# Kernel optimization log

Hardware: AMD Instinct MI355X
Metric: run time of the kernel (lower is better)

Reference implementation:

```python
import jax, jax.numpy as jnp
import numpy as np

N = 50000
E = 800000
IN, HID, OUT = 256, 128, 64
NEG_SLOPE = 0.2


def _gat(x, src, dst, W, a_src, a_dst, b, heads, dim, concat):
    # PyG GATConv (eval mode, self-loops already appended to src/dst)
    xh = (x @ W).reshape(N, heads, dim)              # [N,H,D]
    s_src = jnp.einsum('nhd,hd->nh', xh, a_src)       # [N,H]
    s_dst = jnp.einsum('nhd,hd->nh', xh, a_dst)
    e = jax.nn.leaky_relu(s_src[src] + s_dst[dst], NEG_SLOPE)  # [Etot,H]
    m = jax.ops.segment_max(e, dst, num_segments=N)
    e = jnp.exp(e - m[dst])
    z = jax.ops.segment_sum(e, dst, num_segments=N)
    alpha = e / z[dst]                                # segment softmax over incoming edges
    msg = xh[src] * alpha[:, :, None]                 # [Etot,H,D] gather + weight
    out = jax.ops.segment_sum(msg, dst, num_segments=N)  # scatter-add aggregate
    out = out.reshape(N, heads * dim) if concat else out.mean(axis=1)
    return out + b


def setup_inputs():
    key = jax.random.key(0)
    ks = jax.random.split(key, 20)
    sc = 0.05
    inp = {
        'x': jax.random.normal(ks[0], (N, IN), jnp.float32),
        'edge_index': jax.random.randint(ks[1], (2, E), 0, N, jnp.int64) if jax.config.read('jax_enable_x64') else jax.random.randint(ks[1], (2, E), 0, N, jnp.int32),
        # semantic MLP
        'w1': jax.random.normal(ks[2], (IN, HID), jnp.float32) * sc,
        'b1': jnp.zeros((HID,), jnp.float32),
        'w2': jax.random.normal(ks[3], (HID, HID), jnp.float32) * sc,
        'b2': jnp.zeros((HID,), jnp.float32),
        # gat1: HID -> HID//2, heads=4, concat -> 2*HID
        'g1_w': jax.random.normal(ks[4], (HID, 4 * (HID // 2)), jnp.float32) * sc,
        'g1_asrc': jax.random.normal(ks[5], (4, HID // 2), jnp.float32) * sc,
        'g1_adst': jax.random.normal(ks[6], (4, HID // 2), jnp.float32) * sc,
        'g1_b': jnp.zeros((2 * HID,), jnp.float32),
        # gat2: 2*HID -> OUT, heads=2, mean
        'g2_w': jax.random.normal(ks[7], (2 * HID, 2 * OUT), jnp.float32) * sc,
        'g2_asrc': jax.random.normal(ks[8], (2, OUT), jnp.float32) * sc,
        'g2_adst': jax.random.normal(ks[9], (2, OUT), jnp.float32) * sc,
        'g2_b': jnp.zeros((OUT,), jnp.float32),
        # gat3: OUT -> OUT, heads=1, mean
        'g3_w': jax.random.normal(ks[10], (OUT, OUT), jnp.float32) * sc,
        'g3_asrc': jax.random.normal(ks[11], (1, OUT), jnp.float32) * sc,
        'g3_adst': jax.random.normal(ks[12], (1, OUT), jnp.float32) * sc,
        'g3_b': jnp.zeros((OUT,), jnp.float32),
    }
    return inp


def reference(x, edge_index, w1, b1, w2, b2,
              g1_w, g1_asrc, g1_adst, g1_b,
              g2_w, g2_asrc, g2_adst, g2_b,
              g3_w, g3_asrc, g3_adst, g3_b):
    # add self loops once (PyG GATConv default add_self_loops=True)
    loop = jnp.arange(N, dtype=edge_index.dtype)
    src = jnp.concatenate([edge_index[0], loop])
    dst = jnp.concatenate([edge_index[1], loop])
    # semantic MLP (eval: dropout is identity)
    h = jax.nn.relu(x @ w1 + b1)
    h = jax.nn.relu(h @ w2 + b2)
    h = jax.nn.elu(_gat(h, src, dst, g1_w, g1_asrc, g1_adst, g1_b, 4, HID // 2, True))
    h = jax.nn.elu(_gat(h, src, dst, g2_w, g2_asrc, g2_adst, g2_b, 2, OUT, False))
    h = _gat(h, src, dst, g3_w, g3_asrc, g3_adst, g3_b, 1, OUT, False)
    return h
```

## Files before the change

### kernel.cpp

```cpp
#include <hip/hip_runtime.h>
#include <hip/hip_fp16.h>
#include <math.h>

#define NN 50000
#define NE 800000

static inline int ceil_div_h(int a, int b) { return (a + b - 1) / b; }

typedef _Float16 half8 __attribute__((ext_vector_type(8)));
typedef float f32x4 __attribute__((ext_vector_type(4)));

__global__ __launch_bounds__(256)
void prep_kernel(const float* __restrict__ w1, const float* __restrict__ w2,
                 const float* __restrict__ g1w, const float* __restrict__ g2w,
                 const float* __restrict__ g3w, __half* __restrict__ wt,
                 int* __restrict__ cursor) {
  int idx = blockIdx.x * 256 + threadIdx.x;
  if (idx < NN) cursor[idx] = 0;
  const float* W; int K, N, li;
  if (idx < 32768)        { W = w1;  K = 256; N = 128; li = idx; }
  else if (idx < 49152)   { W = w2;  K = 128; N = 128; li = idx - 32768; }
  else if (idx < 81920)   { W = g1w; K = 128; N = 256; li = idx - 49152; }
  else if (idx < 114688)  { W = g2w; K = 256; N = 128; li = idx - 81920; }
  else if (idx < 118784)  { W = g3w; K = 64;  N = 64;  li = idx - 114688; }
  else return;
  int n = li / K, k = li - n * K;
  wt[idx] = __float2half_rn(W[(size_t)k * N + n]);
}

template<int BM, int TN, int WR, int WC, int ACT, int OUTH, int AF32, int HS>
__global__ __launch_bounds__(256)
void mfma_gemm(const void* __restrict__ Av, const __half* __restrict__ Bt,
               const float* __restrict__ bias, void* __restrict__ Cv,
               const float* __restrict__ a_src, const float* __restrict__ a_dst,
               float* __restrict__ s_src, float* __restrict__ s_dst,
               int M, int N, int K) {
  constexpr int FM = BM / WR / 16;
  constexpr int FN = TN / WC / 16;
  constexpr int SA = 40;
  __shared__ __align__(16) _Float16 As[BM * SA];
  __shared__ __align__(16) _Float16 Bs[TN * SA];
  const int tid = threadIdx.x;
  const int bm = blockIdx.y * BM, bn = blockIdx.x * TN;
  const int wave = tid >> 6, lane = tid & 63;
  const int wm = (wave % WR) * (BM / WR);
  const int wn = (wave / WR) * (TN / WC);
  const int l16 = lane & 15, quad = lane >> 4;

  f32x4 acc[FM][FN] = {};

  for (int k0 = 0; k0 < K; k0 += 32) {
    if (AF32) {
      const float* A = (const float*)Av;
      #pragma unroll
      for (int i = 0; i < (BM * 8) / 256; ++i) {
        int idx = tid + i * 256;
        int m = idx >> 3, q = idx & 7;
        int gm = bm + m;
        float4 v = make_float4(0.f, 0.f, 0.f, 0.f);
        if (gm < M) v = *(const float4*)&A[(size_t)gm * K + k0 + q * 4];
        union { __half2 h2[2]; float2 f2; } u;
        u.h2[0] = __floats2half2_rn(v.x, v.y);
        u.h2[1] = __floats2half2_rn(v.z, v.w);
        *(float2*)&As[m * SA + q * 4] = u.f2;
      }
    } else {
      const __half* A = (const __half*)Av;
      #pragma unroll
      for (int i = 0; i < (BM * 4) / 256; ++i) {
        int idx = tid + i * 256;
        int m = idx >> 2, q = (idx & 3) * 8;
        int gm = bm + m;
        float4 raw = make_float4(0.f, 0.f, 0.f, 0.f);
        if (gm < M) raw = *(const float4*)&A[(size_t)gm * K + k0 + q];
        *(float4*)&As[m * SA + q] = raw;
      }
    }
    #pragma unroll
    for (int i = 0; i < (TN * 4) / 256; ++i) {
      int idx = tid + i * 256;
      int n = idx >> 2, kq = (idx & 3) * 8;
      float4 raw = *(const float4*)&Bt[(size_t)(bn + n) * K + k0 + kq];
      *(float4*)&Bs[n * SA + kq] = raw;
    }
    __syncthreads();
    half8 af[FM], bf[FN];
    #pragma unroll
    for (int mi = 0; mi < FM; ++mi)
      af[mi] = *(const half8*)&As[(wm + mi * 16 + l16) * SA + quad * 8];
    #pragma unroll
    for (int ni = 0; ni < FN; ++ni)
      bf[ni] = *(const half8*)&Bs[(wn + ni * 16 + l16) * SA + quad * 8];
    #pragma unroll
    for (int mi = 0; mi < FM; ++mi)
      #pragma unroll
      for (int ni = 0; ni < FN; ++ni)
        acc[mi][ni] = __builtin_amdgcn_mfma_f32_16x16x32_f16(af[mi], bf[ni], acc[mi][ni], 0, 0, 0);
    __syncthreads();
  }

  #pragma unroll
  for (int mi = 0; mi < FM; ++mi) {
    #pragma unroll
    for (int r = 0; r < 4; ++r) {
      int gm = bm + wm + mi * 16 + quad * 4 + r;
      if (gm >= M) continue;
      #pragma unroll
      for (int ni = 0; ni < FN; ++ni) {
        int gn = bn + wn + ni * 16 + l16;
        float v = acc[mi][ni][r];
        if (bias) v += bias[gn];
        if (ACT == 1) v = fmaxf(v, 0.f);
        if (OUTH) ((__half*)Cv)[(size_t)gm * N + gn] = __float2half_rn(v);
        else      ((float*)Cv)[(size_t)gm * N + gn] = v;
      }
    }
  }

  if (HS > 0) {
    const int h = (bn + wn) >> 6;
    float asv[FN], adv[FN];
    #pragma unroll
    for (int ni = 0; ni < FN; ++ni) {
      int d = ni * 16 + l16;
      asv[ni] = a_src[h * 64 + d];
      adv[ni] = a_dst[h * 64 + d];
    }
    #pragma unroll
    for (int mi = 0; mi < FM; ++mi) {
      #pragma unroll
      for (int r = 0; r < 4; ++r) {
        float ss = 0.f, sd = 0.f;
        #pragma unroll
        for (int ni = 0; ni < FN; ++ni) {
          float v = acc[mi][ni][r];
          ss = fmaf(v, asv[ni], ss);
          sd = fmaf(v, adv[ni], sd);
        }
        #pragma unroll
        for (int off = 1; off < 16; off <<= 1) {
          ss += __shfl_xor(ss, off, 64);
          sd += __shfl_xor(sd, off, 64);
        }
        int gm = bm + wm + mi * 16 + quad * 4 + r;
        if (l16 == 0 && gm < M) {
          s_src[gm * HS + h] = ss;
          s_dst[gm * HS + h] = sd;
        }
      }
    }
  }
}


__global__ __launch_bounds__(256)
void hist_kernel(const int* __restrict__ ei, int* __restrict__ cnt) {
  int e = blockIdx.x * blockDim.x + threadIdx.x;
  if (e >= NE) return;
  atomicAdd(&cnt[ei[NE + e]], 1);
}

__global__ __launch_bounds__(256)
void scan1_kernel(const int* __restrict__ in, int* __restrict__ out,
                  int* __restrict__ bsum, int n) {
  __shared__ int tmp[256];
  int t = threadIdx.x;
  int i = blockIdx.x * 256 + t;
  int v = (i < n) ? in[i] : 0;
  tmp[t] = v;
  __syncthreads();
  for (int off = 1; off < 256; off <<= 1) {
    int u = (t >= off) ? tmp[t - off] : 0;
    __syncthreads();
    tmp[t] += u;
    __syncthreads();
  }
  if (i <= n) out[i] = tmp[t] - v;
  if (t == 255) bsum[blockIdx.x] = tmp[255];
}

__global__ __launch_bounds__(256)
void scan2_kernel(int* __restrict__ data, int n) {
  __shared__ int tmp[256];
  int t = threadIdx.x;
  int v = (t < n) ? data[t] : 0;
  tmp[t] = v;
  __syncthreads();
  for (int off = 1; off < 256; off <<= 1) {
    int u = (t >= off) ? tmp[t - off] : 0;
    __syncthreads();
    tmp[t] += u;
    __syncthreads();
  }
  if (t < n) data[t] = tmp[t] - v;
}

__global__ __launch_bounds__(256)
void scan3_kernel(int* __restrict__ out, const int* __restrict__ bsum,
                  int* __restrict__ cursor, int n) {
  int i = blockIdx.x * 256 + threadIdx.x;
  if (i > n) return;
  int v = out[i] + bsum[blockIdx.x];
  out[i] = v;
  if (i < n) cursor[i] = v;
}

__global__ __launch_bounds__(256)
void scatter_kernel(const int* __restrict__ ei, int* __restrict__ cursor,
                    int* __restrict__ srcs) {
  int e = blockIdx.x * blockDim.x + threadIdx.x;
  if (e >= NE) return;
  int s = ei[e], d = ei[NE + e];
  int pos = atomicAdd(&cursor[d], 1);
  srcs[pos] = s;
}

template<int H, int MODE>
__global__ __launch_bounds__(256)
void gat_aggregate(const int* __restrict__ rowptr, const int* __restrict__ srcs,
                   const float* __restrict__ ssrc, const float* __restrict__ sdst,
                   const __half* __restrict__ xh, const float* __restrict__ bias,
                   void* __restrict__ outv) {
  constexpr int HD = H * 64;
  __shared__ float wbuf[4][64 * H];
  __shared__ int sbuf[4][64];
  const int wslot = threadIdx.x >> 6;
  const int wid = (blockIdx.x * blockDim.x + threadIdx.x) >> 6;
  const int lane = threadIdx.x & 63;
  if (wid >= NN) return;
  const int n = wid;
  const int start = rowptr[n];
  const int end = rowptr[n + 1];
  const int h = (lane * H) >> 6;

  float sdv[H];
  #pragma unroll
  for (int hh = 0; hh < H; ++hh) sdv[hh] = sdst[n * H + hh];

  float z;
  float acc[H];
  {
    float wself[H];
    #pragma unroll
    for (int hh = 0; hh < H; ++hh) {
      float e = ssrc[n * H + hh] + sdv[hh];
      e = e >= 0.f ? e : 0.2f * e;
      wself[hh] = __expf(e);
    }
    float ws = wself[h];
    z = ws;
    const __half* xr = xh + (size_t)n * HD + lane * H;
    if (H == 4) {
      float2 raw = *(const float2*)xr;
      __half2 p0 = *(__half2*)&raw.x;
      __half2 p1 = *(__half2*)&raw.y;
      float2 f0 = __half22float2(p0), f1 = __half22float2(p1);
      acc[0] = ws * f0.x; acc[1] = ws * f0.y; acc[2] = ws * f1.x; acc[3] = ws * f1.y;
    } else if (H == 2) {
      float2 f0 = __half22float2(*(const __half2*)xr);
      acc[0] = ws * f0.x; acc[1] = ws * f0.y;
    } else {
      acc[0] = ws * __half2float(xr[0]);
    }
  }

  for (int base = start; base < end; base += 64) {
    int cnt = end - base;
    if (cnt > 64) cnt = 64;
    if (lane < cnt) {
      int s = srcs[base + lane];
      sbuf[wslot][lane] = s;
      float ev[H];
      if (H == 4) {
        float4 t = *(const float4*)&ssrc[s * 4];
        ev[0] = t.x; ev[1] = t.y; ev[2] = t.z; ev[3] = t.w;
      } else if (H == 2) {
        float2 t = *(const float2*)&ssrc[s * 2];
        ev[0] = t.x; ev[1] = t.y;
      } else {
        ev[0] = ssrc[s];
      }
      #pragma unroll
      for (int hh = 0; hh < H; ++hh) {
        float e = ev[hh] + sdv[hh];
        e = e >= 0.f ? e : 0.2f * e;
        wbuf[wslot][lane * H + hh] = __expf(e);
      }
    }
    #pragma unroll 4
    for (int j = 0; j < cnt; ++j) {
      int s = sbuf[wslot][j];
      float w = wbuf[wslot][j * H + h];
      z += w;
      const __half* xr = xh + (size_t)s * HD + lane * H;
      if (H == 4) {
        float2 raw = *(const float2*)xr;
        __half2 p0 = *(__half2*)&raw.x;
        __half2 p1 = *(__half2*)&raw.y;
        float2 f0 = __half22float2(p0), f1 = __half22float2(p1);
        acc[0] = fmaf(w, f0.x, acc[0]); acc[1] = fmaf(w, f0.y, acc[1]);
        acc[2] = fmaf(w, f1.x, acc[2]); acc[3] = fmaf(w, f1.y, acc[3]);
      } else if (H == 2) {
        float2 f0 = __half22float2(*(const __half2*)xr);
        acc[0] = fmaf(w, f0.x, acc[0]); acc[1] = fmaf(w, f0.y, acc[1]);
      } else {
        acc[0] = fmaf(w, __half2float(xr[0]), acc[0]);
      }
    }
  }
  const float inv = 1.f / z;

  if (MODE == 0) {
    __half* out = (__half*)outv;
    float v[4];
    #pragma unroll
    for (int i = 0; i < 4; ++i) {
      v[i] = acc[i] * inv + bias[lane * 4 + i];
      v[i] = v[i] > 0.f ? v[i] : expm1f(v[i]);
    }
    union { __half2 h2[2]; float2 f2; } u;
    u.h2[0] = __floats2half2_rn(v[0], v[1]);
    u.h2[1] = __floats2half2_rn(v[2], v[3]);
    *(float2*)&out[(size_t)n * 256 + lane * 4] = u.f2;
  } else if (MODE == 1) {
    __half* out = (__half*)outv;
    float sv[2];
    #pragma unroll
    for (int i = 0; i < 2; ++i) {
      float mine = acc[i] * inv;
      float other = __shfl_xor(mine, 32, 64);
      sv[i] = (mine + other) * 0.5f;
    }
    if (lane < 32) {
      float v0 = sv[0] + bias[lane * 2 + 0];
      float v1 = sv[1] + bias[lane * 2 + 1];
      v0 = v0 > 0.f ? v0 : expm1f(v0);
      v1 = v1 > 0.f ? v1 : expm1f(v1);
      *(__half2*)&out[(size_t)n * 64 + lane * 2] = __floats2half2_rn(v0, v1);
    }
  } else {
    float* out = (float*)outv;
    out[(size_t)n * 64 + lane] = acc[0] * inv + bias[lane];
  }
}


extern "C" void kernel_launch(void* const* d_in, const int* in_sizes, int n_in,
                              void* d_out, int out_size, void* d_ws, size_t ws_size,
                              hipStream_t stream) {
  const float* x    = (const float*)d_in[0];
  const int*   ei   = (const int*)d_in[1];
  const float* w1   = (const float*)d_in[2];
  const float* b1   = (const float*)d_in[3];
  const float* w2   = (const float*)d_in[4];
  const float* b2   = (const float*)d_in[5];
  const float* g1w  = (const float*)d_in[6];
  const float* g1as = (const float*)d_in[7];
  const float* g1ad = (const float*)d_in[8];
  const float* g1b  = (const float*)d_in[9];
  const float* g2w  = (const float*)d_in[10];
  const float* g2as = (const float*)d_in[11];
  const float* g2ad = (const float*)d_in[12];
  const float* g2b  = (const float*)d_in[13];
  const float* g3w  = (const float*)d_in[14];
  const float* g3as = (const float*)d_in[15];
  const float* g3ad = (const float*)d_in[16];
  const float* g3b  = (const float*)d_in[17];
  float* out = (float*)d_out;

  float* ws   = (float*)d_ws;
  float* bufA = ws;
  float* bufB = bufA + (size_t)NN * 256;
  float* bufC = bufB + (size_t)NN * 256;
  float* ssrc = bufC + (size_t)NN * 256;
  float* sdst = ssrc + (size_t)NN * 4;
  int* rowptr = (int*)(sdst + (size_t)NN * 4);
  int* cursor = rowptr + (NN + 1);
  int* bsum   = cursor + NN;
  int* srcs   = bsum + 256;
  __half* wt   = (__half*)(srcs + NE);
  __half* wt1  = wt;
  __half* wt2  = wt + 32768;
  __half* wtg1 = wt + 49152;
  __half* wtg2 = wt + 81920;
  __half* wtg3 = wt + 114688;

  __half* h1  = (__half*)bufA;
  __half* h2  = (__half*)bufB;
  __half* xh1 = (__half*)bufC;
  __half* a1  = (__half*)bufA;
  __half* xh2 = (__half*)bufB;
  __half* a2  = (__half*)bufC;
  __half* xh3 = (__half*)bufB;

  const int TB = 256;
  const int grid_m = ceil_div_h(NN, 64);
  const int egrid = ceil_div_h(NE, TB);
  const int sgrid = ceil_div_h(NN + 1, TB);
  const int wgrid = ceil_div_h(NN, 4);

  prep_kernel<<<ceil_div_h(118784, TB), TB, 0, stream>>>(w1, w2, g1w, g2w, g3w, wt, cursor);

  hist_kernel<<<egrid, TB, 0, stream>>>(ei, cursor);
  scan1_kernel<<<sgrid, TB, 0, stream>>>(cursor, rowptr, bsum, NN);
  scan2_kernel<<<1, TB, 0, stream>>>(bsum, sgrid);
  scan3_kernel<<<sgrid, TB, 0, stream>>>(rowptr, bsum, cursor, NN);
  scatter_kernel<<<egrid, TB, 0, stream>>>(ei, cursor, srcs);

  mfma_gemm<64, 128, 2, 2, 1, 1, 1, 0><<<dim3(1, grid_m), TB, 0, stream>>>(
      x, wt1, b1, h1, nullptr, nullptr, nullptr, nullptr, NN, 128, 256);
  mfma_gemm<64, 128, 2, 2, 1, 1, 0, 0><<<dim3(1, grid_m), TB, 0, stream>>>(
      h1, wt2, b2, h2, nullptr, nullptr, nullptr, nullptr, NN, 128, 128);

  mfma_gemm<64, 128, 2, 2, 0, 1, 0, 4><<<dim3(2, grid_m), TB, 0, stream>>>(
      h2, wtg1, nullptr, xh1, g1as, g1ad, ssrc, sdst, NN, 256, 128);
  gat_aggregate<4, 0><<<wgrid, TB, 0, stream>>>(rowptr, srcs, ssrc, sdst, xh1, g1b, a1);

  mfma_gemm<64, 128, 2, 2, 0, 1, 0, 2><<<dim3(1, grid_m), TB, 0, stream>>>(
      a1, wtg2, nullptr, xh2, g2as, g2ad, ssrc, sdst, NN, 128, 256);
  gat_aggregate<2, 1><<<wgrid, TB, 0, stream>>>(rowptr, srcs, ssrc, sdst, xh2, g2b, a2);

  mfma_gemm<64, 64, 4, 1, 0, 1, 0, 1><<<dim3(1, grid_m), TB, 0, stream>>>(
      a2, wtg3, nullptr, xh3, g3as, g3ad, ssrc, sdst, NN, 64, 64);
  gat_aggregate<1, 2><<<wgrid, TB, 0, stream>>>(rowptr, srcs, ssrc, sdst, xh3, g3b, out);
}
```

Before: 417.5 us.

## Fuse MLP layers and GAT1 projection into one kernel with LDS intermediates

Replaces three separate MFMA GEMM launches (x@W1, h1@W2, h2@Wg1 with attention scores) with one kernel per 64-row tile. The h1 and h2 intermediates stay in shared memory as fp16, so they are never written to or read back from global memory, and two launches go away. In exchange each block uses more LDS (about 60KB), which lowers occupancy. The two GEMMs that were separate grids now run sequentially inside each block.

```diff
diff --git a/kernel.cpp b/kernel.cpp
--- a/kernel.cpp
+++ b/kernel.cpp
@@ -26,6 +26,180 @@
   else return;
   int n = li / K, k = li - n * K;
   wt[idx] = __float2half_rn(W[(size_t)k * N + n]);
+}
+
+__global__ __launch_bounds__(256)
+void mlp_gat1_fused(const float* __restrict__ x,
+                    const __half* __restrict__ wt1,
+                    const float* __restrict__ b1,
+                    const __half* __restrict__ wt2,
+                    const float* __restrict__ b2,
+                    const __half* __restrict__ wtg1,
+                    const float* __restrict__ a_src, const float* __restrict__ a_dst,
+                    __half* __restrict__ xh1,
+                    float* __restrict__ s_src, float* __restrict__ s_dst) {
+  constexpr int SA = 40;
+  constexpr int SH = 136;
+  __shared__ __align__(16) _Float16 As[64 * SA];
+  __shared__ __align__(16) _Float16 Bs[256 * SA];
+  __shared__ __align__(16) _Float16 h1s[64 * SH];
+  __shared__ __align__(16) _Float16 h2s[64 * SH];
+  const int tid = threadIdx.x;
+  const int bm = blockIdx.x * 64;
+  const int wave = tid >> 6, lane = tid & 63;
+  const int l16 = lane & 15, quad = lane >> 4;
+  const int wm = (wave & 1) * 32;
+  const int wn = (wave >> 1) * 64;
+
+  {
+    f32x4 acc[2][4] = {};
+    for (int k0 = 0; k0 < 256; k0 += 32) {
+      #pragma unroll
+      for (int i = 0; i < 2; ++i) {
+        int idx = tid + i * 256;
+        int m = idx >> 3, q = idx & 7;
+        int gm = bm + m;
+        float4 v = make_float4(0.f, 0.f, 0.f, 0.f);
+        if (gm < NN) v = *(const float4*)&x[(size_t)gm * 256 + k0 + q * 4];
+        union { __half2 h2[2]; float2 f2; } u;
+        u.h2[0] = __floats2half2_rn(v.x, v.y);
+        u.h2[1] = __floats2half2_rn(v.z, v.w);
+        *(float2*)&As[m * SA + q * 4] = u.f2;
+      }
+      #pragma unroll
+      for (int i = 0; i < 2; ++i) {
+        int idx = tid + i * 256;
+        int n = idx >> 2, kq = (idx & 3) * 8;
+        *(float4*)&Bs[n * SA + kq] = *(const float4*)&wt1[(size_t)n * 256 + k0 + kq];
+      }
+      __syncthreads();
+      half8 af[2], bf[4];
+      #pragma unroll
+      for (int mi = 0; mi < 2; ++mi)
+        af[mi] = *(const half8*)&As[(wm + mi * 16 + l16) * SA + quad * 8];
+      #pragma unroll
+      for (int ni = 0; ni < 4; ++ni)
+        bf[ni] = *(const half8*)&Bs[(wn + ni * 16 + l16) * SA + quad * 8];
+      #pragma unroll
+      for (int mi = 0; mi < 2; ++mi)
+        #pragma unroll
+        for (int ni = 0; ni < 4; ++ni)
+          acc[mi][ni] = __builtin_amdgcn_mfma_f32_16x16x32_f16(af[mi], bf[ni], acc[mi][ni], 0, 0, 0);
+      __syncthreads();
+    }
+    #pragma unroll
+    for (int mi = 0; mi < 2; ++mi)
+      #pragma unroll
+      for (int r = 0; r < 4; ++r) {
+        int row = wm + mi * 16 + quad * 4 + r;
+        #pragma unroll
+        for (int ni = 0; ni < 4; ++ni) {
+          int col = wn + ni * 16 + l16;
+          float v = acc[mi][ni][r] + b1[col];
+          v = fmaxf(v, 0.f);
+          h1s[row * SH + col] = (_Float16)v;
+        }
+      }
+  }
+  __syncthreads();
+
+  {
+    f32x4 acc[2][4] = {};
+    for (int k0 = 0; k0 < 128; k0 += 32) {
+      #pragma unroll
+      for (int i = 0; i < 2; ++i) {
+        int idx = tid + i * 256;
+        int n = idx >> 2, kq = (idx & 3) * 8;
+        *(float4*)&Bs[n * SA + kq] = *(const float4*)&wt2[(size_t)n * 128 + k0 + kq];
+      }
+      __syncthreads();
+      half8 af[2], bf[4];
+      #pragma unroll
+      for (int mi = 0; mi < 2; ++mi)
+        af[mi] = *(const half8*)&h1s[(wm + mi * 16 + l16) * SH + k0 + quad * 8];
+      #pragma unroll
+      for (int ni = 0; ni < 4; ++ni)
+        bf[ni] = *(const half8*)&Bs[(wn + ni * 16 + l16) * SA + quad * 8];
+      #pragma unroll
+      for (int mi = 0; mi < 2; ++mi)
+        #pragma unroll
+        for (int ni = 0; ni < 4; ++ni)
+          acc[mi][ni] = __builtin_amdgcn_mfma_f32_16x16x32_f16(af[mi], bf[ni], acc[mi][ni], 0, 0, 0);
+      __syncthreads();
+    }
+    #pragma unroll
+    for (int mi = 0; mi < 2; ++mi)
+      #pragma unroll
+      for (int r = 0; r < 4; ++r) {
+        int row = wm + mi * 16 + quad * 4 + r;
+        #pragma unroll
+        for (int ni = 0; ni < 4; ++ni) {
+          int col = wn + ni * 16 + l16;
+          float v = acc[mi][ni][r] + b2[col];
+          v = fmaxf(v, 0.f);
+          h2s[row * SH + col] = (_Float16)v;
+        }
+      }
+  }
+  __syncthreads();
+
+  {
+    f32x4 acc[4][4] = {};
+    const int wn3 = wave * 64;
+    for (int k0 = 0; k0 < 128; k0 += 32) {
+      #pragma unroll
+      for (int i = 0; i < 4; ++i) {
+        int idx = tid + i * 256;
+        int n = idx >> 2, kq = (idx & 3) * 8;
+        *(float4*)&Bs[n * SA + kq] = *(const float4*)&wtg1[(size_t)n * 128 + k0 + kq];
+      }
+      __syncthreads();
+      half8 af[4], bf[4];
+      #pragma unroll
+      for (int mi = 0; mi < 4; ++mi)
+        af[mi] = *(const half8*)&h2s[(mi * 16 + l16) * SH + k0 + quad * 8];
+      #pragma unroll
+      for (int ni = 0; ni < 4; ++ni)
+        bf[ni] = *(const half8*)&Bs[(wn3 + ni * 16 + l16) * SA + quad * 8];
+      #pragma unroll
+      for (int mi = 0; mi < 4; ++mi)
+        #pragma unroll
+        for (int ni = 0; ni < 4; ++ni)
+          acc[mi][ni] = __builtin_amdgcn_mfma_f32_16x16x32_f16(af[mi], bf[ni], acc[mi][ni], 0, 0, 0);
+      __syncthreads();
+    }
+    float asv[4], adv[4];
+    #pragma unroll
+    for (int ni = 0; ni < 4; ++ni) {
+      int d = ni * 16 + l16;
+      asv[ni] = a_src[wave * 64 + d];
+      adv[ni] = a_dst[wave * 64 + d];
+    }
+    #pragma unroll
+    for (int mi = 0; mi < 4; ++mi) {
+      #pragma unroll
+      for (int r = 0; r < 4; ++r) {
+        int gm = bm + mi * 16 + quad * 4 + r;
+        float ss = 0.f, sd = 0.f;
+        #pragma unroll
+        for (int ni = 0; ni < 4; ++ni) {
+          float v = acc[mi][ni][r];
+          ss = fmaf(v, asv[ni], ss);
+          sd = fmaf(v, adv[ni], sd);
+          if (gm < NN) xh1[(size_t)gm * 256 + wn3 + ni * 16 + l16] = __float2half_rn(v);
+        }
+        #pragma unroll
+        for (int off = 1; off < 16; off <<= 1) {
+          ss += __shfl_xor(ss, off, 64);
+          sd += __shfl_xor(sd, off, 64);
+        }
+        if (l16 == 0 && gm < NN) {
+          s_src[gm * 4 + wave] = ss;
+          s_dst[gm * 4 + wave] = sd;
+        }
+      }
+    }
+  }
 }
 
 template<int BM, int TN, int WR, int WC, int ACT, int OUTH, int AF32, int HS>
@@ -385,8 +559,6 @@
   __half* wtg2 = wt + 81920;
   __half* wtg3 = wt + 114688;
 
-  __half* h1  = (__half*)bufA;
-  __half* h2  = (__half*)bufB;
   __half* xh1 = (__half*)bufC;
   __half* a1  = (__half*)bufA;
   __half* xh2 = (__half*)bufB;
@@ -407,13 +579,8 @@
   scan3_kernel<<<sgrid, TB, 0, stream>>>(rowptr, bsum, cursor, NN);
   scatter_kernel<<<egrid, TB, 0, stream>>>(ei, cursor, srcs);
 
-  mfma_gemm<64, 128, 2, 2, 1, 1, 1, 0><<<dim3(1, grid_m), TB, 0, stream>>>(
-      x, wt1, b1, h1, nullptr, nullptr, nullptr, nullptr, NN, 128, 256);
-  mfma_gemm<64, 128, 2, 2, 1, 1, 0, 0><<<dim3(1, grid_m), TB, 0, stream>>>(
-      h1, wt2, b2, h2, nullptr, nullptr, nullptr, nullptr, NN, 128, 128);
-
-  mfma_gemm<64, 128, 2, 2, 0, 1, 0, 4><<<dim3(2, grid_m), TB, 0, stream>>>(
-      h2, wtg1, nullptr, xh1, g1as, g1ad, ssrc, sdst, NN, 256, 128);
+  mlp_gat1_fused<<<grid_m, TB, 0, stream>>>(x, wt1, b1, wt2, b2, wtg1,
+                                            g1as, g1ad, xh1, ssrc, sdst);
   gat_aggregate<4, 0><<<wgrid, TB, 0, stream>>>(rowptr, srcs, ssrc, sdst, xh1, g1b, a1);
 
   mfma_gemm<64, 128, 2, 2, 0, 1, 0, 2><<<dim3(1, grid_m), TB, 0, stream>>>(
```

Result: faster. 407.1 us (-2.5%).
